# Kernel optimization log

Hardware: AMD Instinct MI355X
Metric: run time of the kernel (lower is better)

Reference implementation:

```python
import jax, jax.numpy as jnp
import numpy as np

FEATURE_MAPS = [38, 19, 10, 5, 3, 1]
NUM_ANCHORS = [4, 6, 6, 6, 4, 4]
SCALES = (0.2, 0.9)
RATIOS = np.array([1.0, 1.0, 2.0, 3.0, 0.5, 1.0 / 3.0])
BACKGROUND_ID = 0
EPS = 1e-6


def _generate_anchors():
    """Replicates AnchorManager._generate_anchors: order is (i, j, k)."""
    all_anchors = []
    for size, n in zip(FEATURE_MAPS, NUM_ANCHORS):
        scales = np.linspace(SCALES[0], SCALES[1], n)
        ratios = RATIOS[:n]
        rs = np.sqrt(ratios)
        w = scales * rs          # [n]
        h = scales / rs          # [n]
        cy = (np.arange(size) + 0.5) / size  # i -> rows (varies slowest)
        cx = (np.arange(size) + 0.5) / size  # j -> cols
        grid = np.zeros((size, size, n, 4), dtype=np.float64)
        grid[..., 0] = cx[None, :, None]
        grid[..., 1] = cy[:, None, None]
        grid[..., 2] = w[None, None, :]
        grid[..., 3] = h[None, None, :]
        all_anchors.append(grid.reshape(-1, 4))
    return np.concatenate(all_anchors).astype(np.float32)  # [A, 4] cxcywh


def _cxcywh_to_xyxy(b):
    cxy, wh = b[..., :2], b[..., 2:]
    return jnp.concatenate([cxy - wh / 2, cxy + wh / 2], axis=-1)


def _xyxy_to_cxcywh(b):
    xy1, xy2 = b[..., :2], b[..., 2:]
    return jnp.concatenate([(xy1 + xy2) / 2, xy2 - xy1], axis=-1)


def setup_inputs() -> dict:
    key = jax.random.key(0)
    k1, k2, k3 = jax.random.split(key, 3)
    B, N = 64, 100
    # valid normalized xyxy gt boxes
    xy = jax.random.uniform(k1, (B, N, 2), dtype=jnp.float32) * 0.8
    wh = jax.random.uniform(k2, (B, N, 2), dtype=jnp.float32) * 0.19 + 0.01
    gt_boxes = jnp.concatenate([xy, xy + wh], axis=-1)
    gt_labels = jax.random.randint(k3, (B, N), 1, 81, dtype=jnp.int64 if jax.config.jax_enable_x64 else jnp.int32).astype(jnp.int32)
    anchors_cxcywh = jnp.asarray(_generate_anchors())          # [A, 4]
    anchors_xyxy = _cxcywh_to_xyxy(anchors_cxcywh)             # [A, 4]
    return {
        "gt_labels": gt_labels,
        "gt_boxes": gt_boxes,
        "anchors_cxcywh": anchors_cxcywh,
        "anchors_xyxy": anchors_xyxy,
    }


def _iou(anchors_xyxy, gt_boxes):
    # anchors_xyxy: [A,4], gt_boxes: [B,N,4] -> iou [B,A,N]
    a = anchors_xyxy[None, :, None, :]   # [1,A,1,4]
    g = gt_boxes[:, None, :, :]          # [B,1,N,4]
    lt = jnp.maximum(a[..., :2], g[..., :2])
    rb = jnp.minimum(a[..., 2:], g[..., 2:])
    wh = jnp.clip(rb - lt, 0.0)
    inter = wh[..., 0] * wh[..., 1]
    area_a = (a[..., 2] - a[..., 0]) * (a[..., 3] - a[..., 1])
    area_g = (g[..., 2] - g[..., 0]) * (g[..., 3] - g[..., 1])
    return (inter / (area_a + area_g - inter)).astype(jnp.float32)


def reference(gt_labels, gt_boxes, anchors_cxcywh, anchors_xyxy):
    B, N = gt_boxes.shape[0], gt_boxes.shape[1]
    A = anchors_cxcywh.shape[0]

    gt_boxes_coco = _xyxy_to_cxcywh(gt_boxes)                  # [B,N,4]
    ious = _iou(anchors_xyxy, gt_boxes)                        # [B,A,N]

    anchors_gt = jnp.max(ious, axis=-1)                        # [B,A]
    anchors_gt_idx = jnp.argmax(ious, axis=-1)                 # [B,A]
    gt_anchors_idx = jnp.argmax(ious, axis=-2)                 # [B,N] best anchor per gt

    # force-match: each gt claims its best anchor
    b_idx = jnp.arange(B)[:, None]
    range_n = jnp.broadcast_to(jnp.arange(N), (B, N))
    anchors_gt_idx = anchors_gt_idx.at[b_idx, gt_anchors_idx].set(range_n)
    anchors_gt = anchors_gt.at[b_idx, gt_anchors_idx].set(2.0)

    pos_mask = anchors_gt > 0.5                                # [B,A]

    matched_gtb = jnp.take_along_axis(gt_boxes_coco, anchors_gt_idx[..., None], axis=1)  # [B,A,4]
    matched_labels = jnp.take_along_axis(gt_labels, anchors_gt_idx, axis=1)              # [B,A]
    encoded_labels = jnp.where(pos_mask, matched_labels, BACKGROUND_ID)

    anc = anchors_cxcywh[None]                                 # [1,A,4]
    enc_cxy = (matched_gtb[..., :2] - anc[..., :2]) / anc[..., 2:]
    enc_wh = jnp.log((matched_gtb[..., 2:] + EPS) / (anc[..., 2:] + EPS))
    encoded = jnp.concatenate([enc_cxy, enc_wh], axis=-1)      # [B,A,4]

    return encoded_labels, encoded, pos_mask
```

## Files before the change

### kernel.cpp

```cpp
#include <hip/hip_runtime.h>
#include <math.h>

#pragma clang fp contract(off)


#define AA 8732
#define NN 100
#define BB 64
#define NTILE 35
#define EPS_F 1e-6f
#define OVR_FLAG 0x10000
#define POS_BIT  0x8000
#define DEFL 0.9999995f

__constant__ int FM_SIZE[6] = {38, 19, 10, 5, 3, 1};
__constant__ int FM_NF[6]   = {4, 6, 6, 6, 4, 4};
__constant__ int FM_OFF[6]  = {0, 5776, 7942, 8542, 8692, 8728};

__device__ __forceinline__ void geom(const float4 axy, const float4 g,
                                     float area_a, float ag,
                                     float& inter, float& uni) {
    float ltx = fmaxf(axy.x, g.x);
    float lty = fmaxf(axy.y, g.y);
    float rbx = fminf(axy.z, g.z);
    float rby = fminf(axy.w, g.w);
    float w = fmaxf(rbx - ltx, 0.0f);
    float h = fmaxf(rby - lty, 0.0f);
    inter = w * h;
    uni = area_a + ag - inter;
}

__global__ void prior_kernel(const float4* __restrict__ gt_boxes,
                             const float4* __restrict__ anchors_xyxy,
                             unsigned long long* __restrict__ colmax) {
    const int b = blockIdx.x;
    const int n = threadIdx.x;
    if (n >= NN) return;
    float4 g = gt_boxes[b * NN + n];
    float ag = (g.z - g.x) * (g.w - g.y);
    float cx = (g.x + g.z) * 0.5f;
    float cy = (g.y + g.w) * 0.5f;
    float best = 0.0f;
    for (int f = 0; f < 6; f++) {
        int s = FM_SIZE[f];
        int j = (int)(cx * (float)s); j = j < s - 1 ? j : s - 1;
        int i = (int)(cy * (float)s); i = i < s - 1 ? i : s - 1;
        int base = FM_OFF[f] + (i * s + j) * FM_NF[f];
        for (int k = 0; k < FM_NF[f]; k++) {
            float4 an = anchors_xyxy[base + k];
            float area_a = (an.z - an.x) * (an.w - an.y);
            float inter, uni;
            geom(an, g, area_a, ag, inter, uni);
            best = fmaxf(best, inter * __builtin_amdgcn_rcpf(uni));
        }
    }
    float defl = best * DEFL;
    colmax[b * NN + n] = ((unsigned long long)__float_as_uint(defl)) << 32;
}

template <int N0, int N1>
__device__ __forceinline__ void passChunk(
        const float4 axy, const float area_a, const unsigned lowkey,
        const int b, const int tid,
        const float4* __restrict__ sg,
        float2* sac,
        unsigned long long* __restrict__ colmax,
        float& rt, unsigned& rm)
{
    #pragma unroll 4
    for (int n = N0; n < N1; n++) {
        float4 g = sg[n];
        float2 aw = sac[n];
        float inter, uni;
        geom(axy, g, area_a, aw.x, inter, uni);
        float qa = inter * __builtin_amdgcn_rcpf(uni);
        bool r = (qa > 0.0f) && (qa >= rt);
        rt = fmaxf(rt, qa * DEFL);
        rm |= (r ? 1u : 0u) << (n - N0);
        if (__any((int)(qa >= aw.y))) {
            float iou = inter / uni;
            bool cc = (qa >= aw.y);
            unsigned long long p = cc
                ? ((((unsigned long long)__float_as_uint(iou)) << 32) |
                   (unsigned long long)lowkey) : 0ull;
            #pragma unroll
            for (int off = 32; off > 0; off >>= 1) {
                unsigned long long o = __shfl_xor(p, off);
                p = o > p ? o : p;
            }
            if ((tid & 63) == 0 && p != 0ull) {
                atomicMax(colmax + b * NN + n, p);
                atomicMax((unsigned*)&sac[n].y,
                    __float_as_uint(__uint_as_float((unsigned)(p >> 32)) * DEFL));
            }
        }
    }
}

__global__ __launch_bounds__(256) void iou_pass_kernel(
        const float4* __restrict__ gt_boxes,
        const float4* __restrict__ anchors_xyxy,
        unsigned long long* __restrict__ colmax,
        int* __restrict__ out_slot)
{
    const int b = blockIdx.y;
    const int tid = threadIdx.x;
    const int a = blockIdx.x * 256 + tid;
    const bool valid = (a < AA);
    const int ac = valid ? a : (AA - 1);

    __shared__ float4 sg[NN];
    __shared__ float2 sac[NN];

    if (tid < NN) {
        float4 g = gt_boxes[b * NN + tid];
        sg[tid] = g;
        unsigned hi = (unsigned)(colmax[b * NN + tid] >> 32);
        sac[tid] = make_float2((g.z - g.x) * (g.w - g.y),
                               __uint_as_float(hi) * DEFL);
    }
    __syncthreads();

    const float4 axy = anchors_xyxy[ac];
    const float area_a = (axy.z - axy.x) * (axy.w - axy.y);
    const unsigned lowkey = (unsigned)(AA - ac);

    float rt = 0.0f;
    unsigned rm0 = 0, rm1 = 0, rm2 = 0, rm3 = 0;
    passChunk<0, 32>(axy, area_a, lowkey, b, tid, sg, sac, colmax, rt, rm0);
    passChunk<32, 64>(axy, area_a, lowkey, b, tid, sg, sac, colmax, rt, rm1);
    passChunk<64, 96>(axy, area_a, lowkey, b, tid, sg, sac, colmax, rt, rm2);
    passChunk<96, NN>(axy, area_a, lowkey, b, tid, sg, sac, colmax, rt, rm3);

    float bv = 0.0f;
    int bi = 0;
    unsigned rms[4] = {rm0, rm1, rm2, rm3};
    #pragma unroll
    for (int h = 0; h < 4; h++) {
        unsigned m = rms[h];
        const int nb = h * 32;
        while (m) {
            int n = __builtin_ctz(m) + nb;
            m &= m - 1;
            float inter, uni;
            geom(axy, sg[n], area_a, sac[n].x, inter, uni);
            float qa = inter * __builtin_amdgcn_rcpf(uni);
            if (qa > 0.0f && qa >= rt) {
                float iou = inter / uni;
                if (iou > bv) { bv = iou; bi = n; }
            }
        }
    }

    if (valid) {
        out_slot[(size_t)b * AA + a] = bi | (bv > 0.5f ? POS_BIT : 0);
    }
}

__global__ __launch_bounds__(256) void encode_fused_kernel(
        const int* __restrict__ gt_labels,
        const float4* __restrict__ gt_boxes,
        const float4* __restrict__ anchors_cxcywh,
        const unsigned long long* __restrict__ colmax,
        float* __restrict__ out)
{
    const int b = blockIdx.y;
    const int tid = threadIdx.x;
    const int abase = blockIdx.x * 256;

    __shared__ float4 sg[NN];
    __shared__ int    slab[NN];
    __shared__ int    ovr[256];

    ovr[tid] = -1;
    if (tid < NN) {
        sg[tid]   = gt_boxes[b * NN + tid];
        slab[tid] = gt_labels[b * NN + tid];
    }
    __syncthreads();
    if (tid < NN) {
        unsigned long long v = colmax[b * NN + tid];
        unsigned low = (unsigned)(v & 0xFFFFFFFFull);
        if (low >= 1u && low <= (unsigned)AA) {
            int rel = (AA - (int)low) - abase;
            if (rel >= 0 && rel < 256) atomicMax(&ovr[rel], tid);
        }
    }
    __syncthreads();

    const int a = abase + tid;
    if (a >= AA) return;

    const size_t BA = (size_t)BB * AA;
    const size_t base = (size_t)b * AA + a;

    int s = ((const int*)(out + 5 * BA))[base];
    int o = ovr[tid];

    int idx; bool pos;
    if (o >= 0) { idx = o;          pos = true; }
    else        { idx = s & 0x7FFF; pos = (s & POS_BIT) != 0; }

    const float4 g = sg[idx];
    const float gcx = (g.x + g.z) * 0.5f;
    const float gcy = (g.y + g.w) * 0.5f;
    const float gw  = g.z - g.x;
    const float gh  = g.w - g.y;

    const float4 anc = anchors_cxcywh[a];
    const float ecx = (gcx - anc.x) / anc.z;
    const float ecy = (gcy - anc.y) / anc.w;
    const float ew  = logf((gw + EPS_F) / (anc.z + EPS_F));
    const float eh  = logf((gh + EPS_F) / (anc.w + EPS_F));

    out[base] = pos ? (float)slab[idx] : 0.0f;
    ((float4*)(out + BA))[base] = make_float4(ecx, ecy, ew, eh);
    out[5 * BA + base] = pos ? 1.0f : 0.0f;
}

__global__ void scatter_kernel(const unsigned long long* __restrict__ colmax,
                               int* __restrict__ out_slot) {
    const int b = blockIdx.x;
    const int n = threadIdx.x;
    if (n < NN) {
        unsigned long long v = colmax[b * NN + n];
        unsigned low = (unsigned)(v & 0xFFFFFFFFull);
        if (low >= 1u && low <= (unsigned)AA) {
            int idx = AA - (int)low;
            atomicMax(&out_slot[(size_t)b * AA + idx], OVR_FLAG + n);
        }
    }
}

__global__ __launch_bounds__(256) void encode_kernel(
        const int* __restrict__ gt_labels,
        const float4* __restrict__ gt_boxes,
        const float4* __restrict__ anchors_cxcywh,
        float* __restrict__ out)
{
    const int b = blockIdx.y;
    const int tid = threadIdx.x;
    const int a = blockIdx.x * 256 + tid;

    __shared__ float4 sg[NN];
    __shared__ int    slab[NN];
    if (tid < NN) {
        sg[tid]   = gt_boxes[b * NN + tid];
        slab[tid] = gt_labels[b * NN + tid];
    }
    __syncthreads();
    if (a >= AA) return;

    const size_t BA = (size_t)BB * AA;
    const size_t base = (size_t)b * AA + a;

    int s = ((const int*)(out + 5 * BA))[base];

    int idx; bool pos;
    if (s >= OVR_FLAG) { idx = s - OVR_FLAG;  pos = true; }
    else               { idx = s & 0x7FFF;    pos = (s & POS_BIT) != 0; }

    const float4 g = sg[idx];
    const float gcx = (g.x + g.z) * 0.5f;
    const float gcy = (g.y + g.w) * 0.5f;
    const float gw  = g.z - g.x;
    const float gh  = g.w - g.y;

    const float4 anc = anchors_cxcywh[a];
    const float ecx = (gcx - anc.x) / anc.z;
    const float ecy = (gcy - anc.y) / anc.w;
    const float ew  = logf((gw + EPS_F) / (anc.z + EPS_F));
    const float eh  = logf((gh + EPS_F) / (anc.w + EPS_F));

    out[base] = pos ? (float)slab[idx] : 0.0f;
    ((float4*)(out + BA))[base] = make_float4(ecx, ecy, ew, eh);
    out[5 * BA + base] = pos ? 1.0f : 0.0f;
}

extern "C" void kernel_launch(void* const* d_in, const int* in_sizes, int n_in,
                              void* d_out, int out_size, void* d_ws, size_t ws_size,
                              hipStream_t stream) {
    const int*    gt_labels    = (const int*)d_in[0];
    const float4* gt_boxes     = (const float4*)d_in[1];
    const float4* anchors_cxcy = (const float4*)d_in[2];
    const float4* anchors_xyxy = (const float4*)d_in[3];
    float* out = (float*)d_out;

    const size_t BA = (size_t)BB * AA;
    int* slot = (int*)(out + 5 * BA);

    const bool fused = (ws_size >= (size_t)(BB * NN * 8));
    unsigned long long* colmax = fused
        ? (unsigned long long*)d_ws
        : (unsigned long long*)(out + BA);

    prior_kernel<<<BB, 128, 0, stream>>>(gt_boxes, anchors_xyxy, colmax);

    dim3 grid(NTILE, BB);
    iou_pass_kernel<<<grid, 256, 0, stream>>>(gt_boxes, anchors_xyxy,
                                              colmax, slot);
    if (fused) {
        encode_fused_kernel<<<grid, 256, 0, stream>>>(gt_labels, gt_boxes,
                                                      anchors_cxcy, colmax,
                                                      out);
    } else {
        scatter_kernel<<<BB, 128, 0, stream>>>(colmax, slot);
        encode_kernel<<<grid, 256, 0, stream>>>(gt_labels, gt_boxes,
                                                anchors_cxcy, out);
    }
}
```

Before: 128.6 us.

## Split GT dimension across wave quarters with persistent task-slot IoU kernel

Replaces the per-anchor IoU pass with a persistent kernel. Each wavefront handles 16 anchors and splits the 100 ground truths into four chunks of 25 across lane groups, then merges row maxima and argmax with cross-lane shuffles. The per-GT area and column-threshold array now lives in global memory (asq) instead of shared memory, and tasks are spread evenly across a fixed pool of 8192 wave slots. This shortens the serial per-thread loop and raises parallelism, at the cost of global rather than LDS traffic for GT data and more shuffle reductions.

```diff
diff --git a/kernel.cpp b/kernel.cpp
--- a/kernel.cpp
+++ b/kernel.cpp
@@ -7,11 +7,17 @@
 #define AA 8732
 #define NN 100
 #define BB 64
+#define CH 25
+#define AW 16
+#define TILES_PB 546
+#define NTASK (BB * TILES_PB)
+#define NSLOT 8192
 #define NTILE 35
 #define EPS_F 1e-6f
 #define OVR_FLAG 0x10000
 #define POS_BIT  0x8000
 #define DEFL 0.9999995f
+#define RT_SEED 1e-38f
 
 __constant__ int FM_SIZE[6] = {38, 19, 10, 5, 3, 1};
 __constant__ int FM_NF[6]   = {4, 6, 6, 6, 4, 4};
@@ -32,7 +38,8 @@
 
 __global__ void prior_kernel(const float4* __restrict__ gt_boxes,
                              const float4* __restrict__ anchors_xyxy,
-                             unsigned long long* __restrict__ colmax) {
+                             unsigned long long* __restrict__ colmax,
+                             float2* __restrict__ asq) {
     const int b = blockIdx.x;
     const int n = threadIdx.x;
     if (n >= NN) return;
@@ -56,104 +63,101 @@
     }
     float defl = best * DEFL;
     colmax[b * NN + n] = ((unsigned long long)__float_as_uint(defl)) << 32;
-}
-
-template <int N0, int N1>
-__device__ __forceinline__ void passChunk(
-        const float4 axy, const float area_a, const unsigned lowkey,
-        const int b, const int tid,
-        const float4* __restrict__ sg,
-        float2* sac,
-        unsigned long long* __restrict__ colmax,
-        float& rt, unsigned& rm)
-{
-    #pragma unroll 4
-    for (int n = N0; n < N1; n++) {
-        float4 g = sg[n];
-        float2 aw = sac[n];
-        float inter, uni;
-        geom(axy, g, area_a, aw.x, inter, uni);
-        float qa = inter * __builtin_amdgcn_rcpf(uni);
-        bool r = (qa > 0.0f) && (qa >= rt);
-        rt = fmaxf(rt, qa * DEFL);
-        rm |= (r ? 1u : 0u) << (n - N0);
-        if (__any((int)(qa >= aw.y))) {
-            float iou = inter / uni;
-            bool cc = (qa >= aw.y);
-            unsigned long long p = cc
-                ? ((((unsigned long long)__float_as_uint(iou)) << 32) |
-                   (unsigned long long)lowkey) : 0ull;
-            #pragma unroll
-            for (int off = 32; off > 0; off >>= 1) {
-                unsigned long long o = __shfl_xor(p, off);
-                p = o > p ? o : p;
-            }
-            if ((tid & 63) == 0 && p != 0ull) {
-                atomicMax(colmax + b * NN + n, p);
-                atomicMax((unsigned*)&sac[n].y,
-                    __float_as_uint(__uint_as_float((unsigned)(p >> 32)) * DEFL));
-            }
-        }
-    }
-}
-
-__global__ __launch_bounds__(256) void iou_pass_kernel(
+    asq[b * NN + n] = make_float2(ag, defl);
+}
+
+__global__ __launch_bounds__(256, 8) void iou_row_kernel(
         const float4* __restrict__ gt_boxes,
         const float4* __restrict__ anchors_xyxy,
+        float2* __restrict__ asq,
         unsigned long long* __restrict__ colmax,
         int* __restrict__ out_slot)
 {
-    const int b = blockIdx.y;
-    const int tid = threadIdx.x;
-    const int a = blockIdx.x * 256 + tid;
-    const bool valid = (a < AA);
-    const int ac = valid ? a : (AA - 1);
-
-    __shared__ float4 sg[NN];
-    __shared__ float2 sac[NN];
-
-    if (tid < NN) {
-        float4 g = gt_boxes[b * NN + tid];
-        sg[tid] = g;
-        unsigned hi = (unsigned)(colmax[b * NN + tid] >> 32);
-        sac[tid] = make_float2((g.z - g.x) * (g.w - g.y),
-                               __uint_as_float(hi) * DEFL);
-    }
-    __syncthreads();
-
-    const float4 axy = anchors_xyxy[ac];
-    const float area_a = (axy.z - axy.x) * (axy.w - axy.y);
-    const unsigned lowkey = (unsigned)(AA - ac);
-
-    float rt = 0.0f;
-    unsigned rm0 = 0, rm1 = 0, rm2 = 0, rm3 = 0;
-    passChunk<0, 32>(axy, area_a, lowkey, b, tid, sg, sac, colmax, rt, rm0);
-    passChunk<32, 64>(axy, area_a, lowkey, b, tid, sg, sac, colmax, rt, rm1);
-    passChunk<64, 96>(axy, area_a, lowkey, b, tid, sg, sac, colmax, rt, rm2);
-    passChunk<96, NN>(axy, area_a, lowkey, b, tid, sg, sac, colmax, rt, rm3);
-
-    float bv = 0.0f;
-    int bi = 0;
-    unsigned rms[4] = {rm0, rm1, rm2, rm3};
-    #pragma unroll
-    for (int h = 0; h < 4; h++) {
-        unsigned m = rms[h];
-        const int nb = h * 32;
-        while (m) {
-            int n = __builtin_ctz(m) + nb;
-            m &= m - 1;
+    const int tid  = threadIdx.x;
+    const int lane = tid & 63;
+    const int slot = blockIdx.x * 4 + (tid >> 6);
+    const int t0 = (slot * NTASK) >> 13;
+    const int t1 = ((slot + 1) * NTASK) >> 13;
+    const int al = lane & 15;
+    const int c  = lane >> 4;
+    const int n0 = c * CH;
+
+    for (int t = t0; t < t1; t++) {
+        const int b    = t / TILES_PB;
+        const int tile = t - b * TILES_PB;
+        const int a = tile * AW + al;
+        const bool valid = (a < AA);
+        const int ac = valid ? a : (AA - 1);
+        const float4 axy = anchors_xyxy[ac];
+        const float area_a = (axy.z - axy.x) * (axy.w - axy.y);
+        const unsigned lowkey = (unsigned)(AA - ac);
+        const float4* __restrict__ gb = gt_boxes + b * NN;
+        float2* __restrict__ aq = asq + b * NN;
+        unsigned long long* __restrict__ cm = colmax + b * NN;
+
+        float rt = RT_SEED;
+        unsigned rm = 0;
+        #pragma unroll 5
+        for (int i = 0; i < CH; i++) {
+            const int n = n0 + i;
+            float4 g = gb[n];
+            float2 aw = aq[n];
             float inter, uni;
-            geom(axy, sg[n], area_a, sac[n].x, inter, uni);
+            geom(axy, g, area_a, aw.x, inter, uni);
             float qa = inter * __builtin_amdgcn_rcpf(uni);
-            if (qa > 0.0f && qa >= rt) {
+            bool r = (qa >= rt);
+            rt = fmaxf(rt, qa * DEFL);
+            rm |= (r ? 1u : 0u) << i;
+            if (__any((int)(qa >= aw.y))) {
+                float iou = inter / uni;
+                bool cc = (qa >= aw.y);
+                unsigned long long p = cc
+                    ? ((((unsigned long long)__float_as_uint(iou)) << 32) |
+                       (unsigned long long)lowkey) : 0ull;
+                #pragma unroll
+                for (int off = 8; off > 0; off >>= 1) {
+                    unsigned long long o = __shfl_xor(p, off);
+                    p = o > p ? o : p;
+                }
+                if (al == 0 && p != 0ull) {
+                    atomicMax(cm + n, p);
+                    atomicMax((unsigned*)&aq[n].y,
+                        __float_as_uint(
+                            __uint_as_float((unsigned)(p >> 32)) * DEFL));
+                }
+            }
+        }
+
+        rt = fmaxf(rt, __shfl_xor(rt, 16));
+        rt = fmaxf(rt, __shfl_xor(rt, 32));
+
+        float bv = 0.0f;
+        int bi = 0;
+        while (rm) {
+            int i = __builtin_ctz(rm);
+            rm &= rm - 1;
+            int n = n0 + i;
+            float inter, uni;
+            geom(axy, gb[n], area_a, aq[n].x, inter, uni);
+            float qa = inter * __builtin_amdgcn_rcpf(uni);
+            if (qa >= rt) {
                 float iou = inter / uni;
                 if (iou > bv) { bv = iou; bi = n; }
             }
         }
-    }
-
-    if (valid) {
-        out_slot[(size_t)b * AA + a] = bi | (bv > 0.5f ? POS_BIT : 0);
+
+        unsigned long long k =
+            (((unsigned long long)__float_as_uint(bv)) << 32) |
+            (unsigned long long)(unsigned)(NN - bi);
+        unsigned long long o;
+        o = __shfl_xor(k, 16); k = o > k ? o : k;
+        o = __shfl_xor(k, 32); k = o > k ? o : k;
+
+        if (c == 0 && valid) {
+            float fbv = __uint_as_float((unsigned)(k >> 32));
+            int   fbi = NN - (int)(k & 0xFFFFFFFFull);
+            out_slot[(size_t)b * AA + a] = fbi | (fbv > 0.5f ? POS_BIT : 0);
+        }
     }
 }
 
@@ -293,19 +297,23 @@
     unsigned long long* colmax = fused
         ? (unsigned long long*)d_ws
         : (unsigned long long*)(out + BA);
-
-    prior_kernel<<<BB, 128, 0, stream>>>(gt_boxes, anchors_xyxy, colmax);
-
-    dim3 grid(NTILE, BB);
-    iou_pass_kernel<<<grid, 256, 0, stream>>>(gt_boxes, anchors_xyxy,
-                                              colmax, slot);
+    float2* asq = fused
+        ? (float2*)(out + BA)
+        : (float2*)(out + BA + 2 * BB * NN);
+
+    prior_kernel<<<BB, 128, 0, stream>>>(gt_boxes, anchors_xyxy, colmax, asq);
+
+    iou_row_kernel<<<NSLOT / 4, 256, 0, stream>>>(gt_boxes, anchors_xyxy,
+                                                  asq, colmax, slot);
+
+    dim3 egrid(NTILE, BB);
     if (fused) {
-        encode_fused_kernel<<<grid, 256, 0, stream>>>(gt_labels, gt_boxes,
-                                                      anchors_cxcy, colmax,
-                                                      out);
+        encode_fused_kernel<<<egrid, 256, 0, stream>>>(gt_labels, gt_boxes,
+                                                       anchors_cxcy, colmax,
+                                                       out);
     } else {
         scatter_kernel<<<BB, 128, 0, stream>>>(colmax, slot);
-        encode_kernel<<<grid, 256, 0, stream>>>(gt_labels, gt_boxes,
-                                                anchors_cxcy, out);
-    }
-}
+        encode_kernel<<<egrid, 256, 0, stream>>>(gt_labels, gt_boxes,
+                                                 anchors_cxcy, out);
+    }
+}
```

New measurement: 224.9 us. 74.9% more time.

## Replace per-block shared-memory gt table with global precomputed table and global atomics

Applied to the files above, without the earlier changes.

The prior kernel now writes a per-batch global table holding each gt box, its area and its deflated threshold. The IoU pass reads that table directly instead of staging boxes into shared memory, which removes the block-wide barrier and the staging step. Threshold updates become global atomics shared by all blocks of a batch, so tightened thresholds spread across blocks instead of staying inside one. This adds global or L2 latency on every inner-loop load and global atomic traffic. The table is stored in the output buffer and is assumed to be overwritten by the later encode kernel, and the occupancy hint is also raised.

```diff
diff --git a/kernel.cpp b/kernel.cpp
--- a/kernel.cpp
+++ b/kernel.cpp
@@ -12,6 +12,7 @@
 #define OVR_FLAG 0x10000
 #define POS_BIT  0x8000
 #define DEFL 0.9999995f
+#define RT_SEED 1e-38f
 
 __constant__ int FM_SIZE[6] = {38, 19, 10, 5, 3, 1};
 __constant__ int FM_NF[6]   = {4, 6, 6, 6, 4, 4};
@@ -32,7 +33,8 @@
 
 __global__ void prior_kernel(const float4* __restrict__ gt_boxes,
                              const float4* __restrict__ anchors_xyxy,
-                             unsigned long long* __restrict__ colmax) {
+                             unsigned long long* __restrict__ colmax,
+                             float4* __restrict__ tab4) {
     const int b = blockIdx.x;
     const int n = threadIdx.x;
     if (n >= NN) return;
@@ -56,30 +58,32 @@
     }
     float defl = best * DEFL;
     colmax[b * NN + n] = ((unsigned long long)__float_as_uint(defl)) << 32;
+    tab4[(b * NN + n) * 2]     = g;
+    tab4[(b * NN + n) * 2 + 1] = make_float4(ag, defl, 0.0f, 0.0f);
 }
 
 template <int N0, int N1>
 __device__ __forceinline__ void passChunk(
         const float4 axy, const float area_a, const unsigned lowkey,
-        const int b, const int tid,
-        const float4* __restrict__ sg,
-        float2* sac,
-        unsigned long long* __restrict__ colmax,
+        const int tid,
+        const float4* __restrict__ tb,
+        float* tb_at,
+        unsigned long long* __restrict__ cm,
         float& rt, unsigned& rm)
 {
     #pragma unroll 4
     for (int n = N0; n < N1; n++) {
-        float4 g = sg[n];
-        float2 aw = sac[n];
+        float4 g = tb[n * 2];
+        float4 q = tb[n * 2 + 1];
         float inter, uni;
-        geom(axy, g, area_a, aw.x, inter, uni);
+        geom(axy, g, area_a, q.x, inter, uni);
         float qa = inter * __builtin_amdgcn_rcpf(uni);
-        bool r = (qa > 0.0f) && (qa >= rt);
+        bool r = (qa >= rt);
         rt = fmaxf(rt, qa * DEFL);
         rm |= (r ? 1u : 0u) << (n - N0);
-        if (__any((int)(qa >= aw.y))) {
+        if (__any((int)(qa >= q.y))) {
             float iou = inter / uni;
-            bool cc = (qa >= aw.y);
+            bool cc = (qa >= q.y);
             unsigned long long p = cc
                 ? ((((unsigned long long)__float_as_uint(iou)) << 32) |
                    (unsigned long long)lowkey) : 0ull;
@@ -89,17 +93,19 @@
                 p = o > p ? o : p;
             }
             if ((tid & 63) == 0 && p != 0ull) {
-                atomicMax(colmax + b * NN + n, p);
-                atomicMax((unsigned*)&sac[n].y,
-                    __float_as_uint(__uint_as_float((unsigned)(p >> 32)) * DEFL));
+                atomicMax(cm + n, p);
+                atomicMax((unsigned*)(tb_at + n * 8 + 5),
+                    __float_as_uint(
+                        __uint_as_float((unsigned)(p >> 32)) * DEFL));
             }
         }
     }
 }
 
-__global__ __launch_bounds__(256) void iou_pass_kernel(
-        const float4* __restrict__ gt_boxes,
+__global__ __launch_bounds__(256, 8) void iou_smem_kernel(
         const float4* __restrict__ anchors_xyxy,
+        const float4* __restrict__ tab_ro,
+        float* tab_at,
         unsigned long long* __restrict__ colmax,
         int* __restrict__ out_slot)
 {
@@ -109,28 +115,20 @@
     const bool valid = (a < AA);
     const int ac = valid ? a : (AA - 1);
 
-    __shared__ float4 sg[NN];
-    __shared__ float2 sac[NN];
-
-    if (tid < NN) {
-        float4 g = gt_boxes[b * NN + tid];
-        sg[tid] = g;
-        unsigned hi = (unsigned)(colmax[b * NN + tid] >> 32);
-        sac[tid] = make_float2((g.z - g.x) * (g.w - g.y),
-                               __uint_as_float(hi) * DEFL);
-    }
-    __syncthreads();
+    const float4* __restrict__ tb = tab_ro + (size_t)b * NN * 2;
+    float* tbat = tab_at + (size_t)b * NN * 8;
+    unsigned long long* cm = colmax + (size_t)b * NN;
 
     const float4 axy = anchors_xyxy[ac];
     const float area_a = (axy.z - axy.x) * (axy.w - axy.y);
     const unsigned lowkey = (unsigned)(AA - ac);
 
-    float rt = 0.0f;
+    float rt = RT_SEED;
     unsigned rm0 = 0, rm1 = 0, rm2 = 0, rm3 = 0;
-    passChunk<0, 32>(axy, area_a, lowkey, b, tid, sg, sac, colmax, rt, rm0);
-    passChunk<32, 64>(axy, area_a, lowkey, b, tid, sg, sac, colmax, rt, rm1);
-    passChunk<64, 96>(axy, area_a, lowkey, b, tid, sg, sac, colmax, rt, rm2);
-    passChunk<96, NN>(axy, area_a, lowkey, b, tid, sg, sac, colmax, rt, rm3);
+    passChunk<0, 32>(axy, area_a, lowkey, tid, tb, tbat, cm, rt, rm0);
+    passChunk<32, 64>(axy, area_a, lowkey, tid, tb, tbat, cm, rt, rm1);
+    passChunk<64, 96>(axy, area_a, lowkey, tid, tb, tbat, cm, rt, rm2);
+    passChunk<96, NN>(axy, area_a, lowkey, tid, tb, tbat, cm, rt, rm3);
 
     float bv = 0.0f;
     int bi = 0;
@@ -143,9 +141,9 @@
             int n = __builtin_ctz(m) + nb;
             m &= m - 1;
             float inter, uni;
-            geom(axy, sg[n], area_a, sac[n].x, inter, uni);
+            geom(axy, tb[n * 2], area_a, tb[n * 2 + 1].x, inter, uni);
             float qa = inter * __builtin_amdgcn_rcpf(uni);
-            if (qa > 0.0f && qa >= rt) {
+            if (qa >= rt) {
                 float iou = inter / uni;
                 if (iou > bv) { bv = iou; bi = n; }
             }
@@ -293,11 +291,13 @@
     unsigned long long* colmax = fused
         ? (unsigned long long*)d_ws
         : (unsigned long long*)(out + BA);
-
-    prior_kernel<<<BB, 128, 0, stream>>>(gt_boxes, anchors_xyxy, colmax);
+    float* tabf = out + BA + (size_t)BB * NN * 2;
+    float4* tab4 = (float4*)tabf;
+
+    prior_kernel<<<BB, 128, 0, stream>>>(gt_boxes, anchors_xyxy, colmax, tab4);
 
     dim3 grid(NTILE, BB);
-    iou_pass_kernel<<<grid, 256, 0, stream>>>(gt_boxes, anchors_xyxy,
+    iou_smem_kernel<<<grid, 256, 0, stream>>>(anchors_xyxy, tab4, tabf,
                                               colmax, slot);
     if (fused) {
         encode_fused_kernel<<<grid, 256, 0, stream>>>(gt_labels, gt_boxes,
```

Result: slower. 131.4 us (+2.2%).
